# Optimization experiments

Hardware: AMD Instinct MI355X
Metric: run time of the kernel (lower is better)

Reference implementation:

```python
import jax, jax.numpy as jnp
import numpy as np

B, T, DKQ, DV, EKQ, EV, H, OUT = 8, 2048, 64, 64, 128, 128, 4, 32
FF = 4 * EV
NEG = -1e30  # additive mask value (safe stand-in for -inf)


def _ln(x, g, b, eps=1e-5):
    m = x.mean(-1, keepdims=True)
    var = ((x - m) ** 2).mean(-1, keepdims=True)
    return (x - m) * jax.lax.rsqrt(var + eps) * g + b


def _attn(q, k, v, mask):
    # q,k,v: [n, T, E] -> heads [n, H, T, dh]; NOTE: no 1/sqrt(d) scaling (faithful to source)
    n, t, _ = q.shape
    q = q.reshape(n, t, H, -1).transpose(0, 2, 1, 3)
    k = k.reshape(n, t, H, -1).transpose(0, 2, 1, 3)
    v = v.reshape(n, t, H, -1).transpose(0, 2, 1, 3)
    w = jnp.einsum('bhqd,bhkd->bhqk', q, k) + mask  # [n,H,T,T]
    a = jax.nn.softmax(w, axis=-1)
    o = jnp.einsum('bhqk,bhkd->bhqd', a, v)
    return o.transpose(0, 2, 1, 3).reshape(n, t, -1)


def setup_inputs() -> dict:
    key = jax.random.key(0)
    ks = jax.random.split(key, 32)
    w = lambda k, s: jax.random.normal(k, s, jnp.float32) * 0.02
    DIN_A = DKQ + DV
    return {
        'kq': jax.random.normal(ks[0], (B, T, DKQ), jnp.float32),
        'v': jax.random.normal(ks[1], (B, T, DV), jnp.float32),
        # Layer A (input_dim = DKQ+DV, embed = EV)
        'A_Wk': w(ks[2], (DIN_A, EV)), 'A_bk': jnp.zeros((EV,), jnp.float32),
        'A_Wq': w(ks[3], (DIN_A, EV)), 'A_bq': jnp.zeros((EV,), jnp.float32),
        'A_Wv': w(ks[4], (DIN_A, EV)), 'A_bv': jnp.zeros((EV,), jnp.float32),
        'A_f1W': w(ks[5], (EV, FF)), 'A_f1b': jnp.zeros((FF,), jnp.float32),
        'A_f2W': w(ks[6], (FF, EV)), 'A_f2b': jnp.zeros((EV,), jnp.float32),
        'A_n1g': jnp.ones((EV,), jnp.float32), 'A_n1b': jnp.zeros((EV,), jnp.float32),
        'A_n2g': jnp.ones((EV,), jnp.float32), 'A_n2b': jnp.zeros((EV,), jnp.float32),
        # Layer B (kq -> EKQ, vA -> EV)
        'B_Wk': w(ks[7], (DKQ, EKQ)), 'B_bk': jnp.zeros((EKQ,), jnp.float32),
        'B_Wq': w(ks[8], (DKQ, EKQ)), 'B_bq': jnp.zeros((EKQ,), jnp.float32),
        'B_Wv': w(ks[9], (EV, EV)), 'B_bv': jnp.zeros((EV,), jnp.float32),
        'B_f1W': w(ks[10], (EV, FF)), 'B_f1b': jnp.zeros((FF,), jnp.float32),
        'B_f2W': w(ks[11], (FF, EV)), 'B_f2b': jnp.zeros((EV,), jnp.float32),
        # Output head
        'out_W': w(ks[12], (EV, OUT)), 'out_b': jnp.zeros((OUT,), jnp.float32),
    }


def reference(kq, v, A_Wk, A_bk, A_Wq, A_bq, A_Wv, A_bv, A_f1W, A_f1b, A_f2W, A_f2b,
              A_n1g, A_n1b, A_n2g, A_n2b, B_Wk, B_bk, B_Wq, B_bq, B_Wv, B_bv,
              B_f1W, B_f1b, B_f2W, B_f2b, out_W, out_b):
    n, t, _ = kq.shape
    i = jnp.arange(t)[:, None]
    j = jnp.arange(t)[None, :]
    mask_a = jnp.where(j <= i, 0.0, NEG).astype(jnp.float32)               # causal (diag=1)
    mask_b = jnp.where((j < i) | ((i == 0) & (j == 0)), 0.0, NEG).astype(jnp.float32)  # strict causal + (0,0) exception

    # ---- Layer A ----
    X = jnp.concatenate([kq, v], axis=-1)
    K = X @ A_Wk + A_bk
    Q = X @ A_Wq + A_bq
    V = X @ A_Wv + A_bv
    attn_out = _attn(Q, K, V, mask_a)
    h1 = _ln(V + attn_out, A_n1g, A_n1b)
    ff = jax.nn.gelu(h1 @ A_f1W + A_f1b, approximate=False) @ A_f2W + A_f2b
    vA = _ln(h1 + ff, A_n2g, A_n2b)

    # ---- Layer B (no residuals / norms: values is overwritten in source) ----
    K2 = kq @ B_Wk + B_bk
    Q2 = kq @ B_Wq + B_bq
    V2 = vA @ B_Wv + B_bv
    attn_out2 = _attn(Q2, K2, V2, mask_b)
    ff2 = jax.nn.gelu(attn_out2 @ B_f1W + B_f1b, approximate=False) @ B_f2W + B_f2b

    return ff2 @ out_W + out_b
```

## Files before the change

### kernel.cpp

```cpp
#include <hip/hip_runtime.h>
#include <hip/hip_bf16.h>

#define TSEQ 2048
#define NBATCH 8
#define NROWS (NBATCH*TSEQ)
#define EMB 128
#define NH 4
#define DH 32
#define OUTD 32

typedef short s8v __attribute__((ext_vector_type(8)));
typedef float f4v __attribute__((ext_vector_type(4)));

__device__ __forceinline__ unsigned short f2bf(float f){
  unsigned int u = __float_as_uint(f);
  unsigned int r = u + 0x7fffu + ((u >> 16) & 1u);
  return (unsigned short)(r >> 16);
}
__device__ __forceinline__ float bf2f(unsigned short u){
  return __uint_as_float(((unsigned int)u) << 16);
}

struct WPack {
  const float* src[10];
  int off[10];
  int ntk[10];
  int rowoff[10];
  int nsh[10];
  int kn[10];
};
__global__ __launch_bounds__(256) void prep_w(WPack p, short* __restrict__ warena){
  int blk = blockIdx.x, m = 0;
  #pragma unroll
  for (int i=0;i<10;i++){
    int nb = p.kn[i] >> 8;
    if (blk < nb){ m = i; break; }
    blk -= nb;
  }
  int idx = blk*256 + threadIdx.x;
  float x = p.src[m][idx];
  int nsh = p.nsh[m];
  int n = idx & ((1<<nsh)-1);
  int k = idx >> nsh;
  int K = p.kn[m] >> nsh;
  unsigned short hi = f2bf(x);
  unsigned short lo = f2bf(x - bf2f(hi));
  short* dh = warena + p.off[m] + (size_t)(p.rowoff[m] + n)*K + k;
  dh[0]        = (short)hi;
  dh[p.ntk[m]] = (short)lo;
}

struct GOuts {
  const float* bias[3];
  float* of[3];
  unsigned short* ob[3];
};
__global__ __launch_bounds__(256) void gemm2(
    const float* __restrict__ A0, const float* __restrict__ A1,
    const unsigned short* __restrict__ Ab,
    int asplit, int lda0, int lda1, int K, int niter,
    const short* __restrict__ wt, int NTK,
    GOuts og, int NT, int nseg, int act){
  __shared__ short As[2][2][64*40];
  const int tid  = threadIdx.x;
  const int w    = tid >> 6;
  const int lane = tid & 63;
  const int col  = lane & 15;
  const int quad = lane >> 4;
  const int row0 = blockIdx.x * 64;
  const int colg = blockIdx.y*64 + w*16 + col;
  const bool abf = (Ab != nullptr);

  f4v acc[4];
  #pragma unroll
  for (int i=0;i<4;i++) acc[i] = (f4v){0.f,0.f,0.f,0.f};

  const int ar = tid >> 2, ac = (tid & 3)*8;

  float4 pa0, pa1;
  s8v pab;
  if (!abf){
    const int kcol = ac;
    const float* src = (kcol < asplit) ? A0 + (size_t)(row0+ar)*lda0 + kcol
                                       : A1 + (size_t)(row0+ar)*lda1 + (kcol - asplit);
    pa0 = *(const float4*)src; pa1 = *(const float4*)(src+4);
  } else {
    pab = *(const s8v*)(Ab + (size_t)(row0+ar)*K + ac);
  }

  for (int i=0;i<niter;i++){
    const int buf = i & 1;
    if (!abf){
      float xs[8] = {pa0.x,pa0.y,pa0.z,pa0.w,pa1.x,pa1.y,pa1.z,pa1.w};
      s8v hi, lo;
      #pragma unroll
      for (int j=0;j<8;j++){
        unsigned short h = f2bf(xs[j]);
        hi[j] = (short)h;
        lo[j] = (short)f2bf(xs[j] - bf2f(h));
      }
      *(s8v*)&As[buf][0][ar*40 + ac] = hi;
      *(s8v*)&As[buf][1][ar*40 + ac] = lo;
    } else {
      *(s8v*)&As[buf][0][ar*40 + ac] = pab;
    }
    __syncthreads();
    if (i+1 < niter){
      const int kcol = (i+1)*32 + ac;
      if (!abf){
        const float* src = (kcol < asplit) ? A0 + (size_t)(row0+ar)*lda0 + kcol
                                           : A1 + (size_t)(row0+ar)*lda1 + (kcol - asplit);
        pa0 = *(const float4*)src; pa1 = *(const float4*)(src+4);
      } else {
        pab = *(const s8v*)(Ab + (size_t)(row0+ar)*K + kcol);
      }
    }
    const int k0 = i*32;
    const short* wp = wt + (size_t)colg*K + k0 + quad*8;
    s8v bh = *(const s8v*)wp;
    s8v bl = *(const s8v*)(wp + NTK);
    #pragma unroll
    for (int rt=0;rt<4;rt++){
      s8v ah = *(const s8v*)&As[buf][0][(rt*16 + col)*40 + quad*8];
      acc[rt] = __builtin_amdgcn_mfma_f32_16x16x32_bf16(ah, bh, acc[rt], 0, 0, 0);
      if (!abf){
        s8v al = *(const s8v*)&As[buf][1][(rt*16 + col)*40 + quad*8];
        acc[rt] = __builtin_amdgcn_mfma_f32_16x16x32_bf16(al, bh, acc[rt], 0, 0, 0);
      }
      acc[rt] = __builtin_amdgcn_mfma_f32_16x16x32_bf16(ah, bl, acc[rt], 0, 0, 0);
    }
  }

  int seg, lcol, ldc;
  if (nseg > 1){ seg = colg >> 7; lcol = colg & 127; ldc = 128; }
  else         { seg = 0; lcol = colg; ldc = NT; }
  const float bv = og.bias[seg][lcol];
  float* of = og.of[seg];
  unsigned short* ob = og.ob[seg];
  #pragma unroll
  for (int rt=0;rt<4;rt++){
    #pragma unroll
    for (int r=0;r<4;r++){
      const int row = row0 + rt*16 + quad*4 + r;
      float val = acc[rt][r] + bv;
      if (act == 1) val = 0.5f*val*(1.f + erff(val*0.70710678118654752440f));
      if (ob) ob[(size_t)row*ldc + lcol] = f2bf(val);
      else    of[(size_t)row*ldc + lcol] = val;
    }
  }
}

__global__ __launch_bounds__(256) void vtrans(const float* __restrict__ V, unsigned short* __restrict__ Vtb){
  __shared__ short Lt[64*40];
  const int tid = threadIdx.x;
  const int t0 = blockIdx.x * 64;
  const int bh = blockIdx.y;
  const int b = bh >> 2, h = bh & 3;
  {
    const int r = tid >> 2, c = (tid & 3)*8;
    const float* src = V + (size_t)(b*TSEQ + t0 + r)*EMB + h*DH + c;
    float4 x0 = *(const float4*)src;
    float4 x1 = *(const float4*)(src + 4);
    s8v kb;
    kb[0]=(short)f2bf(x0.x); kb[1]=(short)f2bf(x0.y); kb[2]=(short)f2bf(x0.z); kb[3]=(short)f2bf(x0.w);
    kb[4]=(short)f2bf(x1.x); kb[5]=(short)f2bf(x1.y); kb[6]=(short)f2bf(x1.z); kb[7]=(short)f2bf(x1.w);
    *(s8v*)&Lt[r*40 + c] = kb;
  }
  __syncthreads();
  const int d = tid >> 3, kc = (tid & 7)*8;
  s8v o;
  #pragma unroll
  for (int j=0;j<8;j++) o[j] = Lt[(kc + j)*40 + d];
  *(s8v*)(Vtb + ((size_t)bh*32 + d)*TSEQ + t0 + kc) = o;
}

#define KT_STRIDE 40
#define VT_STRIDE 72
#define PW_STRIDE 72
__global__ __launch_bounds__(128) void flash2(const unsigned short* __restrict__ Qb,
                                              const unsigned short* __restrict__ Kb,
                                              const unsigned short* __restrict__ Vtb,
                                              float* __restrict__ O, int mode){
  __shared__ short Kt[64*KT_STRIDE];
  __shared__ short Vt[32*VT_STRIDE];
  __shared__ short Pw[2][16*PW_STRIDE];
  const int tid  = threadIdx.x;
  const int w    = tid >> 6;
  const int lane = tid & 63;
  const int col  = lane & 15;
  const int quad = lane >> 4;
  const int bh = blockIdx.y;
  const int b = bh >> 2, h = bh & 3;
  const int kr = tid >> 1, kc16 = (tid & 1)*16;
  const int vd = tid >> 2, vk16 = (tid & 3)*16;

  for (int pass = 0; pass < 2; pass++){
    const int t = pass ? blockIdx.x : (63 - blockIdx.x);
    const int qbase = t*32 + w*16;
    const int jtmax = t >> 1;

    s8v qf = *(const s8v*)(Qb + (size_t)(b*TSEQ + qbase + col)*EMB + h*DH + quad*8);
    f4v o0 = {0.f,0.f,0.f,0.f}, o1 = {0.f,0.f,0.f,0.f};
    float lr[4] = {0.f,0.f,0.f,0.f};

    s8v ka, kb2, va, vb;
    {
      const unsigned short* kp = Kb + (size_t)(b*TSEQ + kr)*EMB + h*DH + kc16;
      ka = *(const s8v*)kp; kb2 = *(const s8v*)(kp + 8);
      const unsigned short* vp = Vtb + ((size_t)bh*32 + vd)*TSEQ + vk16;
      va = *(const s8v*)vp; vb = *(const s8v*)(vp + 8);
    }

    for (int jt = 0; jt <= jtmax; jt++){
      __syncthreads();
      *(s8v*)&Kt[kr*KT_STRIDE + kc16]     = ka;
      *(s8v*)&Kt[kr*KT_STRIDE + kc16 + 8] = kb2;
      *(s8v*)&Vt[vd*VT_STRIDE + vk16]     = va;
      *(s8v*)&Vt[vd*VT_STRIDE + vk16 + 8] = vb;
      __syncthreads();
      if (jt < jtmax){
        const unsigned short* kp = Kb + (size_t)(b*TSEQ + (jt+1)*64 + kr)*EMB + h*DH + kc16;
        ka = *(const s8v*)kp; kb2 = *(const s8v*)(kp + 8);
        const unsigned short* vp = Vtb + ((size_t)bh*32 + vd)*TSEQ + (jt+1)*64 + vk16;
        va = *(const s8v*)vp; vb = *(const s8v*)(vp + 8);
      }

      f4v s[4];
      #pragma unroll
      for (int t4=0;t4<4;t4++){
        s8v kf = *(const s8v*)&Kt[(t4*16 + col)*KT_STRIDE + quad*8];
        f4v z = {0.f,0.f,0.f,0.f};
        s[t4] = __builtin_amdgcn_mfma_f32_16x16x32_bf16(qf, kf, z, 0, 0, 0);
      }
      if (jt == jtmax){
        const int j0 = jt*64;
        #pragma unroll
        for (int t4=0;t4<4;t4++){
          const int jg = j0 + t4*16 + col;
          #pragma unroll
          for (int r=0;r<4;r++){
            const int qg = qbase + quad*4 + r;
            const bool ok = (mode==0) ? (jg <= qg) : ((jg < qg) || (qg==0 && jg==0));
            s[t4][r] = ok ? s[t4][r] : -1e30f;
          }
        }
      }
      #pragma unroll
      for (int t4=0;t4<4;t4++){
        #pragma unroll
        for (int r=0;r<4;r++){
          float pv = __expf(s[t4][r]);
          s[t4][r] = pv;
          lr[r] += pv;
          Pw[w][(quad*4+r)*PW_STRIDE + t4*16 + col] = (short)f2bf(pv);
        }
      }
      #pragma unroll
      for (int kk=0;kk<2;kk++){
        s8v pf  = *(const s8v*)&Pw[w][col*PW_STRIDE + kk*32 + quad*8];
        s8v vf0 = *(const s8v*)&Vt[(col)*VT_STRIDE    + kk*32 + quad*8];
        s8v vf1 = *(const s8v*)&Vt[(16+col)*VT_STRIDE + kk*32 + quad*8];
        o0 = __builtin_amdgcn_mfma_f32_16x16x32_bf16(pf, vf0, o0, 0, 0, 0);
        o1 = __builtin_amdgcn_mfma_f32_16x16x32_bf16(pf, vf1, o1, 0, 0, 0);
      }
    }
    float* obase = O + (size_t)(b*TSEQ + qbase)*EMB + h*DH;
    #pragma unroll
    for (int r=0;r<4;r++){
      float l = lr[r];
      l += __shfl_xor(l,1); l += __shfl_xor(l,2);
      l += __shfl_xor(l,4); l += __shfl_xor(l,8);
      const float inv = 1.f / l;
      obase[(size_t)(quad*4+r)*EMB + col]      = o0[r]*inv;
      obase[(size_t)(quad*4+r)*EMB + 16 + col] = o1[r]*inv;
    }
  }
}

__global__ __launch_bounds__(64) void ln_res(const float* __restrict__ X, const float* __restrict__ R,
                                             const float* __restrict__ g, const float* __restrict__ bt,
                                             float* __restrict__ out){
  const int row = blockIdx.x;
  const int tid = threadIdx.x;
  const float* xr = X + (size_t)row*EMB;
  const float* rr = R + (size_t)row*EMB;
  float x0 = xr[tid]    + rr[tid];
  float x1 = xr[tid+64] + rr[tid+64];
  float s  = x0 + x1;
  float s2 = x0*x0 + x1*x1;
  #pragma unroll
  for (int off=1; off<64; off<<=1){
    s  += __shfl_xor(s,  off);
    s2 += __shfl_xor(s2, off);
  }
  float mean = s * (1.f/128.f);
  float var  = s2 * (1.f/128.f) - mean*mean;
  float rstd = rsqrtf(var + 1e-5f);
  out[(size_t)row*EMB + tid]    = (x0-mean)*rstd*g[tid]    + bt[tid];
  out[(size_t)row*EMB + tid+64] = (x1-mean)*rstd*g[tid+64] + bt[tid+64];
}

__global__ __launch_bounds__(256) void out_proj(const float* __restrict__ A,
                                                const float* __restrict__ W, const float* __restrict__ bb,
                                                float* __restrict__ out){
  __shared__ float As[8*128];
  __shared__ float Ws2[128*32];
  const int tid = threadIdx.x;
  const int row0 = blockIdx.x * 8;
  for (int idx = tid; idx < 8*128; idx += 256) As[idx] = A[(size_t)row0*128 + idx];
  for (int idx = tid; idx < 128*32; idx += 256) Ws2[idx] = W[idx];
  __syncthreads();
  const int r = tid >> 5, c = tid & 31;
  float acc = bb[c];
  #pragma unroll 8
  for (int k=0;k<128;k++) acc = fmaf(As[r*128 + k], Ws2[k*32 + c], acc);
  out[(size_t)(row0 + r)*OUTD + c] = acc;
}

extern "C" void kernel_launch(void* const* d_in, const int* in_sizes, int n_in,
                              void* d_out, int out_size, void* d_ws, size_t ws_size,
                              hipStream_t stream) {
  const float* kq    = (const float*)d_in[0];
  const float* v     = (const float*)d_in[1];
  const float* A_Wk  = (const float*)d_in[2];  const float* A_bk  = (const float*)d_in[3];
  const float* A_Wq  = (const float*)d_in[4];  const float* A_bq  = (const float*)d_in[5];
  const float* A_Wv  = (const float*)d_in[6];  const float* A_bv  = (const float*)d_in[7];
  const float* A_f1W = (const float*)d_in[8];  const float* A_f1b = (const float*)d_in[9];
  const float* A_f2W = (const float*)d_in[10]; const float* A_f2b = (const float*)d_in[11];
  const float* A_n1g = (const float*)d_in[12]; const float* A_n1b = (const float*)d_in[13];
  const float* A_n2g = (const float*)d_in[14]; const float* A_n2b = (const float*)d_in[15];
  const float* B_Wk  = (const float*)d_in[16]; const float* B_bk  = (const float*)d_in[17];
  const float* B_Wq  = (const float*)d_in[18]; const float* B_bq  = (const float*)d_in[19];
  const float* B_Wv  = (const float*)d_in[20]; const float* B_bv  = (const float*)d_in[21];
  const float* B_f1W = (const float*)d_in[22]; const float* B_f1b = (const float*)d_in[23];
  const float* B_f2W = (const float*)d_in[24]; const float* B_f2b = (const float*)d_in[25];
  const float* out_W = (const float*)d_in[26]; const float* out_b = (const float*)d_in[27];
  float* out = (float*)d_out;
  (void)in_sizes; (void)n_in; (void)out_size; (void)ws_size;

  char* ws = (char*)d_ws;
  const size_t MB = 1024*1024;
  short* warena = (short*)ws;
  float* Vf   = (float*)(ws + 2*MB);
  float* Obuf = (float*)(ws + 10*MB);
  unsigned short* Vtb = (unsigned short*)(ws + 18*MB);
  float* h1   = (float*)(ws + 22*MB);
  unsigned short* mid = (unsigned short*)(ws + 30*MB);
  float* ffo  = (float*)(ws + 46*MB);
  float* vA   = (float*)(ws + 54*MB);
  unsigned short* Qbf = (unsigned short*)(ws + 62*MB);
  unsigned short* Kbf = (unsigned short*)(ws + 66*MB);

  WPack p;
  const float* srcs[10] = {A_Wq,A_Wk,A_Wv,A_f1W,A_f2W,B_Wq,B_Wk,B_Wv,B_f1W,B_f2W};
  int kn[10]     = {16384,16384,16384,65536,65536,8192,8192,16384,65536,65536};
  int nsh[10]    = {7,7,7,9,7,7,7,7,9,7};
  int off[10]    = {0,0,0,98304,229376,360448,360448,393216,425984,557056};
  int ntk[10]    = {49152,49152,49152,65536,65536,16384,16384,16384,65536,65536};
  int rowoff[10] = {0,128,256,0,0,0,128,0,0,0};
  int nblk = 0;
  for (int i=0;i<10;i++){
    p.src[i]=srcs[i]; p.kn[i]=kn[i]; p.nsh[i]=nsh[i];
    p.off[i]=off[i]; p.ntk[i]=ntk[i]; p.rowoff[i]=rowoff[i];
    nblk += kn[i] >> 8;
  }
  prep_w<<<nblk, 256, 0, stream>>>(p, warena);

  GOuts oQKVA = {{A_bq,A_bk,A_bv},{nullptr,nullptr,Vf},{Qbf,Kbf,nullptr}};
  GOuts oF1A  = {{A_f1b,nullptr,nullptr},{nullptr,nullptr,nullptr},{mid,nullptr,nullptr}};
  GOuts oF2A  = {{A_f2b,nullptr,nullptr},{ffo,nullptr,nullptr},{nullptr,nullptr,nullptr}};
  GOuts oQKB  = {{B_bq,B_bk,nullptr},{nullptr,nullptr,nullptr},{Qbf,Kbf,nullptr}};
  GOuts oVB   = {{B_bv,nullptr,nullptr},{Vf,nullptr,nullptr},{nullptr,nullptr,nullptr}};
  GOuts oF1B  = {{B_f1b,nullptr,nullptr},{nullptr,nullptr,nullptr},{mid,nullptr,nullptr}};
  GOuts oF2B  = {{B_f2b,nullptr,nullptr},{ffo,nullptr,nullptr},{nullptr,nullptr,nullptr}};

  gemm2<<<dim3(256,6), 256, 0, stream>>>(kq, v, nullptr, 64, 64, 64, 128, 4,
                                         warena + 0, 49152, oQKVA, 384, 3, 0);
  vtrans<<<dim3(32,32), 256, 0, stream>>>(Vf, Vtb);
  flash2<<<dim3(32,32), 128, 0, stream>>>(Qbf, Kbf, Vtb, Obuf, 0);
  ln_res<<<NROWS, 64, 0, stream>>>(Vf, Obuf, A_n1g, A_n1b, h1);
  gemm2<<<dim3(256,8), 256, 0, stream>>>(h1, h1, nullptr, 128, 128, 128, 128, 4,
                                         warena + 98304, 65536, oF1A, 512, 1, 1);
  gemm2<<<dim3(256,2), 256, 0, stream>>>(nullptr, nullptr, mid, 0, 0, 0, 512, 16,
                                         warena + 229376, 65536, oF2A, 128, 1, 0);
  ln_res<<<NROWS, 64, 0, stream>>>(h1, ffo, A_n2g, A_n2b, vA);

  gemm2<<<dim3(256,4), 256, 0, stream>>>(kq, kq, nullptr, 64, 64, 64, 64, 2,
                                         warena + 360448, 16384, oQKB, 256, 2, 0);
  gemm2<<<dim3(256,2), 256, 0, stream>>>(vA, vA, nullptr, 128, 128, 128, 128, 4,
                                         warena + 393216, 16384, oVB, 128, 1, 0);
  vtrans<<<dim3(32,32), 256, 0, stream>>>(Vf, Vtb);
  flash2<<<dim3(32,32), 128, 0, stream>>>(Qbf, Kbf, Vtb, Obuf, 1);
  gemm2<<<dim3(256,8), 256, 0, stream>>>(Obuf, Obuf, nullptr, 128, 128, 128, 128, 4,
                                         warena + 425984, 65536, oF1B, 512, 1, 1);
  gemm2<<<dim3(256,2), 256, 0, stream>>>(nullptr, nullptr, mid, 0, 0, 0, 512, 16,
                                         warena + 557056, 65536, oF2B, 128, 1, 0);

  out_proj<<<NROWS/8, 256, 0, stream>>>(ffo, out_W, out_b, out);
}
```

Before: 316.1 us.

## Split flash attention over key tiles and pre-split activations into bf16 hi/lo planes

```diff
diff --git a/kernel.cpp b/kernel.cpp
--- a/kernel.cpp
+++ b/kernel.cpp
@@ -8,6 +8,7 @@
 #define NH 4
 #define DH 32
 #define OUTD 32
+#define APLANE (NROWS*EMB)
 
 typedef short s8v __attribute__((ext_vector_type(8)));
 typedef float f4v __attribute__((ext_vector_type(4)));
@@ -50,15 +51,23 @@
   dh[p.ntk[m]] = (short)lo;
 }
 
+__global__ __launch_bounds__(256) void xsplit(const float* __restrict__ kq, const float* __restrict__ v,
+                                              unsigned short* __restrict__ X){
+  int idx = blockIdx.x*256 + threadIdx.x;
+  int row = idx >> 7, c = idx & 127;
+  float val = (c < 64) ? kq[row*64 + c] : v[row*64 + (c-64)];
+  unsigned short hi = f2bf(val);
+  X[idx]          = hi;
+  X[idx + APLANE] = f2bf(val - bf2f(hi));
+}
+
 struct GOuts {
   const float* bias[3];
   float* of[3];
   unsigned short* ob[3];
 };
 __global__ __launch_bounds__(256) void gemm2(
-    const float* __restrict__ A0, const float* __restrict__ A1,
-    const unsigned short* __restrict__ Ab,
-    int asplit, int lda0, int lda1, int K, int niter,
+    const unsigned short* __restrict__ A, int aplane, int lda, int K, int niter,
     const short* __restrict__ wt, int NTK,
     GOuts og, int NT, int nseg, int act){
   __shared__ short As[2][2][64*40];
@@ -69,61 +78,37 @@
   const int quad = lane >> 4;
   const int row0 = blockIdx.x * 64;
   const int colg = blockIdx.y*64 + w*16 + col;
-  const bool abf = (Ab != nullptr);
+  const bool two = (aplane != 0);
 
   f4v acc[4];
   #pragma unroll
   for (int i=0;i<4;i++) acc[i] = (f4v){0.f,0.f,0.f,0.f};
 
   const int ar = tid >> 2, ac = (tid & 3)*8;
-
-  float4 pa0, pa1;
-  s8v pab;
-  if (!abf){
-    const int kcol = ac;
-    const float* src = (kcol < asplit) ? A0 + (size_t)(row0+ar)*lda0 + kcol
-                                       : A1 + (size_t)(row0+ar)*lda1 + (kcol - asplit);
-    pa0 = *(const float4*)src; pa1 = *(const float4*)(src+4);
-  } else {
-    pab = *(const s8v*)(Ab + (size_t)(row0+ar)*K + ac);
-  }
+  const unsigned short* abase = A + (size_t)(row0 + ar)*lda;
+
+  s8v pah, pal;
+  pah = *(const s8v*)(abase + ac);
+  if (two) pal = *(const s8v*)(abase + aplane + ac);
 
   for (int i=0;i<niter;i++){
     const int buf = i & 1;
-    if (!abf){
-      float xs[8] = {pa0.x,pa0.y,pa0.z,pa0.w,pa1.x,pa1.y,pa1.z,pa1.w};
-      s8v hi, lo;
-      #pragma unroll
-      for (int j=0;j<8;j++){
-        unsigned short h = f2bf(xs[j]);
-        hi[j] = (short)h;
-        lo[j] = (short)f2bf(xs[j] - bf2f(h));
-      }
-      *(s8v*)&As[buf][0][ar*40 + ac] = hi;
-      *(s8v*)&As[buf][1][ar*40 + ac] = lo;
-    } else {
-      *(s8v*)&As[buf][0][ar*40 + ac] = pab;
-    }
+    *(s8v*)&As[buf][0][ar*40 + ac] = pah;
+    if (two) *(s8v*)&As[buf][1][ar*40 + ac] = pal;
     __syncthreads();
     if (i+1 < niter){
       const int kcol = (i+1)*32 + ac;
-      if (!abf){
-        const float* src = (kcol < asplit) ? A0 + (size_t)(row0+ar)*lda0 + kcol
-                                           : A1 + (size_t)(row0+ar)*lda1 + (kcol - asplit);
-        pa0 = *(const float4*)src; pa1 = *(const float4*)(src+4);
-      } else {
-        pab = *(const s8v*)(Ab + (size_t)(row0+ar)*K + kcol);
-      }
+      pah = *(const s8v*)(abase + kcol);
+      if (two) pal = *(const s8v*)(abase + aplane + kcol);
     }
-    const int k0 = i*32;
-    const short* wp = wt + (size_t)colg*K + k0 + quad*8;
+    const short* wp = wt + (size_t)colg*K + i*32 + quad*8;
     s8v bh = *(const s8v*)wp;
     s8v bl = *(const s8v*)(wp + NTK);
     #pragma unroll
     for (int rt=0;rt<4;rt++){
       s8v ah = *(const s8v*)&As[buf][0][(rt*16 + col)*40 + quad*8];
       acc[rt] = __builtin_amdgcn_mfma_f32_16x16x32_bf16(ah, bh, acc[rt], 0, 0, 0);
-      if (!abf){
+      if (two){
         s8v al = *(const s8v*)&As[buf][1][(rt*16 + col)*40 + quad*8];
         acc[rt] = __builtin_amdgcn_mfma_f32_16x16x32_bf16(al, bh, acc[rt], 0, 0, 0);
       }
@@ -177,10 +162,12 @@
 #define KT_STRIDE 40
 #define VT_STRIDE 72
 #define PW_STRIDE 72
-__global__ __launch_bounds__(128) void flash2(const unsigned short* __restrict__ Qb,
+__global__ __launch_bounds__(128) void flash3(const unsigned short* __restrict__ Qb,
                                               const unsigned short* __restrict__ Kb,
                                               const unsigned short* __restrict__ Vtb,
-                                              float* __restrict__ O, int mode){
+                                              float* __restrict__ O0, float* __restrict__ O1,
+                                              float* __restrict__ L0, float* __restrict__ L1,
+                                              int mode){
   __shared__ short Kt[64*KT_STRIDE];
   __shared__ short Vt[32*VT_STRIDE];
   __shared__ short Pw[2][16*PW_STRIDE];
@@ -191,6 +178,9 @@
   const int quad = lane >> 4;
   const int bh = blockIdx.y;
   const int b = bh >> 2, h = bh & 3;
+  const int par = blockIdx.z;
+  float* Op = par ? O1 : O0;
+  float* Lp = par ? L1 : L0;
   const int kr = tid >> 1, kc16 = (tid & 1)*16;
   const int vd = tid >> 2, vk16 = (tid & 3)*16;
 
@@ -203,89 +193,93 @@
     f4v o0 = {0.f,0.f,0.f,0.f}, o1 = {0.f,0.f,0.f,0.f};
     float lr[4] = {0.f,0.f,0.f,0.f};
 
-    s8v ka, kb2, va, vb;
-    {
-      const unsigned short* kp = Kb + (size_t)(b*TSEQ + kr)*EMB + h*DH + kc16;
-      ka = *(const s8v*)kp; kb2 = *(const s8v*)(kp + 8);
-      const unsigned short* vp = Vtb + ((size_t)bh*32 + vd)*TSEQ + vk16;
-      va = *(const s8v*)vp; vb = *(const s8v*)(vp + 8);
-    }
-
-    for (int jt = 0; jt <= jtmax; jt++){
-      __syncthreads();
-      *(s8v*)&Kt[kr*KT_STRIDE + kc16]     = ka;
-      *(s8v*)&Kt[kr*KT_STRIDE + kc16 + 8] = kb2;
-      *(s8v*)&Vt[vd*VT_STRIDE + vk16]     = va;
-      *(s8v*)&Vt[vd*VT_STRIDE + vk16 + 8] = vb;
-      __syncthreads();
-      if (jt < jtmax){
-        const unsigned short* kp = Kb + (size_t)(b*TSEQ + (jt+1)*64 + kr)*EMB + h*DH + kc16;
+    if (par <= jtmax){
+      s8v ka, kb2, va, vb;
+      {
+        const unsigned short* kp = Kb + (size_t)(b*TSEQ + par*64 + kr)*EMB + h*DH + kc16;
         ka = *(const s8v*)kp; kb2 = *(const s8v*)(kp + 8);
-        const unsigned short* vp = Vtb + ((size_t)bh*32 + vd)*TSEQ + (jt+1)*64 + vk16;
+        const unsigned short* vp = Vtb + ((size_t)bh*32 + vd)*TSEQ + par*64 + vk16;
         va = *(const s8v*)vp; vb = *(const s8v*)(vp + 8);
       }
-
-      f4v s[4];
-      #pragma unroll
-      for (int t4=0;t4<4;t4++){
-        s8v kf = *(const s8v*)&Kt[(t4*16 + col)*KT_STRIDE + quad*8];
-        f4v z = {0.f,0.f,0.f,0.f};
-        s[t4] = __builtin_amdgcn_mfma_f32_16x16x32_bf16(qf, kf, z, 0, 0, 0);
-      }
-      if (jt == jtmax){
-        const int j0 = jt*64;
+      for (int jt = par; jt <= jtmax; jt += 2){
+        __syncthreads();
+        *(s8v*)&Kt[kr*KT_STRIDE + kc16]     = ka;
+        *(s8v*)&Kt[kr*KT_STRIDE + kc16 + 8] = kb2;
+        *(s8v*)&Vt[vd*VT_STRIDE + vk16]     = va;
+        *(s8v*)&Vt[vd*VT_STRIDE + vk16 + 8] = vb;
+        __syncthreads();
+        if (jt + 2 <= jtmax){
+          const unsigned short* kp = Kb + (size_t)(b*TSEQ + (jt+2)*64 + kr)*EMB + h*DH + kc16;
+          ka = *(const s8v*)kp; kb2 = *(const s8v*)(kp + 8);
+          const unsigned short* vp = Vtb + ((size_t)bh*32 + vd)*TSEQ + (jt+2)*64 + vk16;
+          va = *(const s8v*)vp; vb = *(const s8v*)(vp + 8);
+        }
+        f4v s[4];
         #pragma unroll
         for (int t4=0;t4<4;t4++){
-          const int jg = j0 + t4*16 + col;
+          s8v kf = *(const s8v*)&Kt[(t4*16 + col)*KT_STRIDE + quad*8];
+          f4v z = {0.f,0.f,0.f,0.f};
+          s[t4] = __builtin_amdgcn_mfma_f32_16x16x32_bf16(qf, kf, z, 0, 0, 0);
+        }
+        if (jt == jtmax){
+          const int j0 = jt*64;
+          #pragma unroll
+          for (int t4=0;t4<4;t4++){
+            const int jg = j0 + t4*16 + col;
+            #pragma unroll
+            for (int r=0;r<4;r++){
+              const int qg = qbase + quad*4 + r;
+              const bool ok = (mode==0) ? (jg <= qg) : ((jg < qg) || (qg==0 && jg==0));
+              s[t4][r] = ok ? s[t4][r] : -1e30f;
+            }
+          }
+        }
+        #pragma unroll
+        for (int t4=0;t4<4;t4++){
           #pragma unroll
           for (int r=0;r<4;r++){
-            const int qg = qbase + quad*4 + r;
-            const bool ok = (mode==0) ? (jg <= qg) : ((jg < qg) || (qg==0 && jg==0));
-            s[t4][r] = ok ? s[t4][r] : -1e30f;
+            float pv = __expf(s[t4][r]);
+            s[t4][r] = pv;
+            lr[r] += pv;
+            Pw[w][(quad*4+r)*PW_STRIDE + t4*16 + col] = (short)f2bf(pv);
           }
         }
-      }
-      #pragma unroll
-      for (int t4=0;t4<4;t4++){
         #pragma unroll
-        for (int r=0;r<4;r++){
-          float pv = __expf(s[t4][r]);
-          s[t4][r] = pv;
-          lr[r] += pv;
-          Pw[w][(quad*4+r)*PW_STRIDE + t4*16 + col] = (short)f2bf(pv);
+        for (int kk=0;kk<2;kk++){
+          s8v pf  = *(const s8v*)&Pw[w][col*PW_STRIDE + kk*32 + quad*8];
+          s8v vf0 = *(const s8v*)&Vt[(col)*VT_STRIDE    + kk*32 + quad*8];
+          s8v vf1 = *(const s8v*)&Vt[(16+col)*VT_STRIDE + kk*32 + quad*8];
+          o0 = __builtin_amdgcn_mfma_f32_16x16x32_bf16(pf, vf0, o0, 0, 0, 0);
+          o1 = __builtin_amdgcn_mfma_f32_16x16x32_bf16(pf, vf1, o1, 0, 0, 0);
         }
       }
-      #pragma unroll
-      for (int kk=0;kk<2;kk++){
-        s8v pf  = *(const s8v*)&Pw[w][col*PW_STRIDE + kk*32 + quad*8];
-        s8v vf0 = *(const s8v*)&Vt[(col)*VT_STRIDE    + kk*32 + quad*8];
-        s8v vf1 = *(const s8v*)&Vt[(16+col)*VT_STRIDE + kk*32 + quad*8];
-        o0 = __builtin_amdgcn_mfma_f32_16x16x32_bf16(pf, vf0, o0, 0, 0, 0);
-        o1 = __builtin_amdgcn_mfma_f32_16x16x32_bf16(pf, vf1, o1, 0, 0, 0);
-      }
     }
-    float* obase = O + (size_t)(b*TSEQ + qbase)*EMB + h*DH;
+    float* obase = Op + (size_t)(b*TSEQ + qbase)*EMB + h*DH;
     #pragma unroll
     for (int r=0;r<4;r++){
       float l = lr[r];
       l += __shfl_xor(l,1); l += __shfl_xor(l,2);
       l += __shfl_xor(l,4); l += __shfl_xor(l,8);
-      const float inv = 1.f / l;
-      obase[(size_t)(quad*4+r)*EMB + col]      = o0[r]*inv;
-      obase[(size_t)(quad*4+r)*EMB + 16 + col] = o1[r]*inv;
+      obase[(size_t)(quad*4+r)*EMB + col]      = o0[r];
+      obase[(size_t)(quad*4+r)*EMB + 16 + col] = o1[r];
+      if (col == 0) Lp[(size_t)(b*TSEQ + qbase + quad*4 + r)*NH + h] = l;
     }
   }
 }
 
-__global__ __launch_bounds__(64) void ln_res(const float* __restrict__ X, const float* __restrict__ R,
-                                             const float* __restrict__ g, const float* __restrict__ bt,
-                                             float* __restrict__ out){
+__global__ __launch_bounds__(64) void combine_ln(const float* __restrict__ O0, const float* __restrict__ O1,
+                                                 const float* __restrict__ L0, const float* __restrict__ L1,
+                                                 const float* __restrict__ Vf,
+                                                 const float* __restrict__ g, const float* __restrict__ bt,
+                                                 unsigned short* __restrict__ outp){
   const int row = blockIdx.x;
   const int tid = threadIdx.x;
-  const float* xr = X + (size_t)row*EMB;
-  const float* rr = R + (size_t)row*EMB;
-  float x0 = xr[tid]    + rr[tid];
-  float x1 = xr[tid+64] + rr[tid+64];
+  const size_t base = (size_t)row*EMB;
+  const int h0 = tid >> 5, h1i = 2 + (tid >> 5);
+  const float la = L0[(size_t)row*NH + h0] + L1[(size_t)row*NH + h0];
+  const float lb = L0[(size_t)row*NH + h1i] + L1[(size_t)row*NH + h1i];
+  float x0 = Vf[base+tid]    + (O0[base+tid]    + O1[base+tid])    / la;
+  float x1 = Vf[base+tid+64] + (O0[base+tid+64] + O1[base+tid+64]) / lb;
   float s  = x0 + x1;
   float s2 = x0*x0 + x1*x1;
   #pragma unroll
@@ -296,8 +290,52 @@
   float mean = s * (1.f/128.f);
   float var  = s2 * (1.f/128.f) - mean*mean;
   float rstd = rsqrtf(var + 1e-5f);
-  out[(size_t)row*EMB + tid]    = (x0-mean)*rstd*g[tid]    + bt[tid];
-  out[(size_t)row*EMB + tid+64] = (x1-mean)*rstd*g[tid+64] + bt[tid+64];
+  float y0 = (x0-mean)*rstd*g[tid]    + bt[tid];
+  float y1 = (x1-mean)*rstd*g[tid+64] + bt[tid+64];
+  unsigned short h0b = f2bf(y0), h1b = f2bf(y1);
+  outp[base+tid]             = h0b;
+  outp[base+tid+64]          = h1b;
+  outp[base+tid+APLANE]      = f2bf(y0 - bf2f(h0b));
+  outp[base+tid+64+APLANE]   = f2bf(y1 - bf2f(h1b));
+}
+
+__global__ __launch_bounds__(64) void ln2(const unsigned short* __restrict__ Xp, const float* __restrict__ R,
+                                          const float* __restrict__ g, const float* __restrict__ bt,
+                                          unsigned short* __restrict__ outp){
+  const int row = blockIdx.x;
+  const int tid = threadIdx.x;
+  const size_t base = (size_t)row*EMB;
+  float x0 = bf2f(Xp[base+tid])    + bf2f(Xp[base+tid+APLANE])    + R[base+tid];
+  float x1 = bf2f(Xp[base+tid+64]) + bf2f(Xp[base+tid+64+APLANE]) + R[base+tid+64];
+  float s  = x0 + x1;
+  float s2 = x0*x0 + x1*x1;
+  #pragma unroll
+  for (int off=1; off<64; off<<=1){
+    s  += __shfl_xor(s,  off);
+    s2 += __shfl_xor(s2, off);
+  }
+  float mean = s * (1.f/128.f);
+  float var  = s2 * (1.f/128.f) - mean*mean;
+  float rstd = rsqrtf(var + 1e-5f);
+  float y0 = (x0-mean)*rstd*g[tid]    + bt[tid];
+  float y1 = (x1-mean)*rstd*g[tid+64] + bt[tid+64];
+  unsigned short h0b = f2bf(y0), h1b = f2bf(y1);
+  outp[base+tid]             = h0b;
+  outp[base+tid+64]          = h1b;
+  outp[base+tid+APLANE]      = f2bf(y0 - bf2f(h0b));
+  outp[base+tid+64+APLANE]   = f2bf(y1 - bf2f(h1b));
+}
+
+__global__ __launch_bounds__(256) void combine_b(const float* __restrict__ O0, const float* __restrict__ O1,
+                                                 const float* __restrict__ L0, const float* __restrict__ L1,
+                                                 unsigned short* __restrict__ outp){
+  const int idx = blockIdx.x*256 + threadIdx.x;
+  const int row = idx >> 7, c = idx & 127, h = c >> 5;
+  const float l = L0[(size_t)row*NH + h] + L1[(size_t)row*NH + h];
+  const float v = (O0[idx] + O1[idx]) / l;
+  unsigned short hb = f2bf(v);
+  outp[idx]          = hb;
+  outp[idx + APLANE] = f2bf(v - bf2f(hb));
 }
 
 __global__ __launch_bounds__(256) void out_proj(const float* __restrict__ A,
@@ -341,15 +379,19 @@
   char* ws = (char*)d_ws;
   const size_t MB = 1024*1024;
   short* warena = (short*)ws;
-  float* Vf   = (float*)(ws + 2*MB);
-  float* Obuf = (float*)(ws + 10*MB);
+  unsigned short* Xs  = (unsigned short*)(ws + 2*MB);
+  unsigned short* Qbf = (unsigned short*)(ws + 10*MB);
+  unsigned short* Kbf = (unsigned short*)(ws + 14*MB);
   unsigned short* Vtb = (unsigned short*)(ws + 18*MB);
-  float* h1   = (float*)(ws + 22*MB);
-  unsigned short* mid = (unsigned short*)(ws + 30*MB);
-  float* ffo  = (float*)(ws + 46*MB);
-  float* vA   = (float*)(ws + 54*MB);
-  unsigned short* Qbf = (unsigned short*)(ws + 62*MB);
-  unsigned short* Kbf = (unsigned short*)(ws + 66*MB);
+  float* Vf  = (float*)(ws + 22*MB);
+  float* O0  = (float*)(ws + 30*MB);
+  float* O1  = (float*)(ws + 38*MB);
+  float* L0  = (float*)(ws + 46*MB);
+  float* L1  = (float*)(ws + 47*MB);
+  unsigned short* h1p = (unsigned short*)(ws + 48*MB);
+  unsigned short* mid = (unsigned short*)(ws + 56*MB);
+  float* ffo = (float*)(ws + 72*MB);
+  unsigned short* vAp = (unsigned short*)(ws + 80*MB);
 
   WPack p;
   const float* srcs[10] = {A_Wq,A_Wk,A_Wv,A_f1W,A_f2W,B_Wq,B_Wk,B_Wv,B_f1W,B_f2W};
@@ -365,6 +407,7 @@
     nblk += kn[i] >> 8;
   }
   prep_w<<<nblk, 256, 0, stream>>>(p, warena);
+  xsplit<<<NROWS*128/256, 256, 0, stream>>>(kq, v, Xs);
 
   GOuts oQKVA = {{A_bq,A_bk,A_bv},{nullptr,nullptr,Vf},{Qbf,Kbf,nullptr}};
   GOuts oF1A  = {{A_f1b,nullptr,nullptr},{nullptr,nullptr,nullptr},{mid,nullptr,nullptr}};
@@ -374,27 +417,21 @@
   GOuts oF1B  = {{B_f1b,nullptr,nullptr},{nullptr,nullptr,nullptr},{mid,nullptr,nullptr}};
   GOuts oF2B  = {{B_f2b,nullptr,nullptr},{ffo,nullptr,nullptr},{nullptr,nullptr,nullptr}};
 
-  gemm2<<<dim3(256,6), 256, 0, stream>>>(kq, v, nullptr, 64, 64, 64, 128, 4,
-                                         warena + 0, 49152, oQKVA, 384, 3, 0);
+  gemm2<<<dim3(256,6), 256, 0, stream>>>(Xs, APLANE, 128, 128, 4, warena + 0,      49152, oQKVA, 384, 3, 0);
   vtrans<<<dim3(32,32), 256, 0, stream>>>(Vf, Vtb);
-  flash2<<<dim3(32,32), 128, 0, stream>>>(Qbf, Kbf, Vtb, Obuf, 0);
-  ln_res<<<NROWS, 64, 0, stream>>>(Vf, Obuf, A_n1g, A_n1b, h1);
-  gemm2<<<dim3(256,8), 256, 0, stream>>>(h1, h1, nullptr, 128, 128, 128, 128, 4,
-                                         warena + 98304, 65536, oF1A, 512, 1, 1);
-  gemm2<<<dim3(256,2), 256, 0, stream>>>(nullptr, nullptr, mid, 0, 0, 0, 512, 16,
-                                         warena + 229376, 65536, oF2A, 128, 1, 0);
-  ln_res<<<NROWS, 64, 0, stream>>>(h1, ffo, A_n2g, A_n2b, vA);
-
-  gemm2<<<dim3(256,4), 256, 0, stream>>>(kq, kq, nullptr, 64, 64, 64, 64, 2,
-                                         warena + 360448, 16384, oQKB, 256, 2, 0);
-  gemm2<<<dim3(256,2), 256, 0, stream>>>(vA, vA, nullptr, 128, 128, 128, 128, 4,
-                                         warena + 393216, 16384, oVB, 128, 1, 0);
+  flash3<<<dim3(32,32,2), 128, 0, stream>>>(Qbf, Kbf, Vtb, O0, O1, L0, L1, 0);
+  combine_ln<<<NROWS, 64, 0, stream>>>(O0, O1, L0, L1, Vf, A_n1g, A_n1b, h1p);
+  gemm2<<<dim3(256,8), 256, 0, stream>>>(h1p, APLANE, 128, 128, 4, warena + 98304, 65536, oF1A, 512, 1, 1);
+  gemm2<<<dim3(256,2), 256, 0, stream>>>(mid, 0,      512, 512, 16, warena + 229376, 65536, oF2A, 128, 1, 0);
+  ln2<<<NROWS, 64, 0, stream>>>(h1p, ffo, A_n2g, A_n2b, vAp);
+
+  gemm2<<<dim3(256,4), 256, 0, stream>>>(Xs, APLANE, 128, 64, 2,  warena + 360448, 16384, oQKB, 256, 2, 0);
+  gemm2<<<dim3(256,2), 256, 0, stream>>>(vAp, APLANE, 128, 128, 4, warena + 393216, 16384, oVB, 128, 1, 0);
   vtrans<<<dim3(32,32), 256, 0, stream>>>(Vf, Vtb);
-  flash2<<<dim3(32,32), 128, 0, stream>>>(Qbf, Kbf, Vtb, Obuf, 1);
-  gemm2<<<dim3(256,8), 256, 0, stream>>>(Obuf, Obuf, nullptr, 128, 128, 128, 128, 4,
-                                         warena + 425984, 65536, oF1B, 512, 1, 1);
-  gemm2<<<dim3(256,2), 256, 0, stream>>>(nullptr, nullptr, mid, 0, 0, 0, 512, 16,
-                                         warena + 557056, 65536, oF2B, 128, 1, 0);
+  flash3<<<dim3(32,32,2), 128, 0, stream>>>(Qbf, Kbf, Vtb, O0, O1, L0, L1, 1);
+  combine_b<<<NROWS*128/256, 256, 0, stream>>>(O0, O1, L0, L1, h1p);
+  gemm2<<<dim3(256,8), 256, 0, stream>>>(h1p, APLANE, 128, 128, 4, warena + 425984, 65536, oF1B, 512, 1, 1);
+  gemm2<<<dim3(256,2), 256, 0, stream>>>(mid, 0,      512, 512, 16, warena + 557056, 65536, oF2B, 128, 1, 0);
 
   out_proj<<<NROWS/8, 256, 0, stream>>>(ffo, out_W, out_b, out);
 }
```

After: 313.5 us. No clear change (-0.8%).
